# Kernel optimization log

Measured on AMD Instinct MI355X. Metric: run time of the kernel, lower is better.

Reference implementation:

```python
import jax, jax.numpy as jnp
import numpy as np

D_MODEL = 1024
NUM_HEADS = 16
HEAD_DIM = D_MODEL // NUM_HEADS


def setup_inputs() -> dict:
    key = jax.random.key(0)
    ks = jax.random.split(key, 5)
    scale = 0.02
    return {
        "x": jax.random.normal(ks[0], (1, 4096, D_MODEL), dtype=jnp.float32),
        "w_qkv": jax.random.normal(ks[1], (D_MODEL, 3 * D_MODEL), dtype=jnp.float32) * scale,
        "b_qkv": jax.random.normal(ks[2], (3 * D_MODEL,), dtype=jnp.float32) * scale,
        "w_out": jax.random.normal(ks[3], (D_MODEL, D_MODEL), dtype=jnp.float32) * scale,
        "b_out": jax.random.normal(ks[4], (D_MODEL,), dtype=jnp.float32) * scale,
    }


def reference(x, w_qkv, b_qkv, w_out, b_out):
    B, S, D = x.shape
    H, Hd = NUM_HEADS, HEAD_DIM
    qkv = x @ w_qkv + b_qkv  # [B,S,3D]
    q, k, v = jnp.split(qkv, 3, axis=-1)
    # [B,H,S,Hd]
    q = q.reshape(B, S, H, Hd).transpose(0, 2, 1, 3)
    k = k.reshape(B, S, H, Hd).transpose(0, 2, 1, 3)
    v = v.reshape(B, S, H, Hd).transpose(0, 2, 1, 3)
    scores = jnp.einsum("bhqd,bhkd->bhqk", q, k) / jnp.sqrt(jnp.float32(Hd))
    causal = jnp.tril(jnp.ones((S, S), dtype=bool))
    scores = jnp.where(causal[None, None, :, :], scores, -jnp.inf)
    attn = jax.nn.softmax(scores, axis=-1)  # dropout_p = 0.0 -> identity
    ctx = jnp.einsum("bhqk,bhkd->bhqd", attn, v)
    ctx = ctx.transpose(0, 2, 1, 3).reshape(B, S, D)
    return ctx @ w_out + b_out
```

## Files before the change

kernel.cpp:

```cpp
#include <hip/hip_runtime.h>

#define S 4096
#define DM 1024
#define NH 16
#define HD 64

typedef __attribute__((ext_vector_type(8))) short bf8;
typedef __attribute__((ext_vector_type(4))) float f4;
typedef __attribute__((ext_vector_type(4))) short s4;

#define MFMA __builtin_amdgcn_mfma_f32_16x16x32_bf16

#define QSCALE 0.18033688011112042f

static __device__ __forceinline__ unsigned short f2b(float f) {
  unsigned int u = __builtin_bit_cast(unsigned int, f);
  u += 0x7fffu + ((u >> 16) & 1u);
  return (unsigned short)(u >> 16);
}
static __device__ __forceinline__ float b2f(unsigned short u) {
  return __builtin_bit_cast(float, (unsigned int)u << 16);
}

static __device__ __forceinline__ void gld_lds(const unsigned short* g, unsigned short* l) {
  __builtin_amdgcn_global_load_lds(
      (const __attribute__((address_space(1))) unsigned int*)g,
      (__attribute__((address_space(3))) unsigned int*)l, 16, 0, 0);
}

__global__ void prep(const float* __restrict__ x, const float* __restrict__ w_qkv,
                     const float* __restrict__ w_out,
                     unsigned short* __restrict__ xb, unsigned short* __restrict__ wqkvT,
                     unsigned short* __restrict__ woutT) {
  __shared__ float tile[64][65];
  int b = blockIdx.x, t = threadIdx.x;
  if (b < 4096) {
    int i = (b * 256 + t) * 4;
    float4 v = *(const float4*)(x + i);
    s4 o;
    o.x = (short)f2b(v.x); o.y = (short)f2b(v.y);
    o.z = (short)f2b(v.z); o.w = (short)f2b(v.w);
    *(s4*)(xb + i) = o;
    return;
  }
  const float* in; unsigned short* out; int R, C, tc, tr;
  if (b < 4096 + 768) { int bb = b - 4096; in = w_qkv; out = wqkvT; R = DM; C = 3 * DM; tc = bb % 48; tr = bb / 48; }
  else                { int bb = b - 4864; in = w_out; out = woutT; R = DM; C = DM;     tc = bb % 16; tr = bb / 16; }
  int c = t & 63, rbase = (t >> 6) * 16;
#pragma unroll
  for (int i = 0; i < 16; i++) {
    int r = rbase + i;
    tile[r][c] = in[(tr * 64 + r) * C + tc * 64 + c];
  }
  __syncthreads();
#pragma unroll
  for (int i = 0; i < 16; i++) {
    int cc = rbase + i;
    out[(tc * 64 + cc) * R + tr * 64 + c] = f2b(tile[c][cc]);
  }
}


__global__ void __launch_bounds__(256, 2) gemm_qkv(const unsigned short* __restrict__ A,
                                                   const unsigned short* __restrict__ Bt,
                                                   const float* __restrict__ bias,
                                                   unsigned short* __restrict__ Qo,
                                                   unsigned short* __restrict__ Ko,
                                                   unsigned short* __restrict__ Vt) {
  __shared__ unsigned short lA[128 * 32];
  __shared__ unsigned short lB[128 * 32];
  int bid = blockIdx.x;
  int nb = bid % 24, mb = bid / 24;
  int m0 = mb * 128, n0 = nb * 128;
  int t = threadIdx.x, w = t >> 6, lane = t & 63;
  int col = lane & 15, quad = lane >> 4;
  int wm = (w >> 1) * 64, wn = (w & 1) * 64;

  int srow = lane >> 2;
  int sphys = lane & 3;

  f4 acc[4][4];
#pragma unroll
  for (int x = 0; x < 4; x++)
#pragma unroll
    for (int y = 0; y < 4; y++) acc[x][y] = (f4){0.f, 0.f, 0.f, 0.f};

  for (int k0 = 0; k0 < DM; k0 += 32) {
    __syncthreads();
#pragma unroll
    for (int p = 0; p < 2; p++) {
      int j = 2 * w + p;
      int row = j * 16 + srow;
      int lch = sphys ^ ((srow >> 1) & 3);
      gld_lds(A + (size_t)(m0 + row) * DM + k0 + lch * 8, lA + j * 512);
      gld_lds(Bt + (size_t)(n0 + row) * DM + k0 + lch * 8, lB + j * 512);
    }
    __syncthreads();

    bf8 af[4], bfr[4];
#pragma unroll
    for (int x = 0; x < 4; x++) {
      int rA = wm + x * 16 + col;
      af[x] = *(const bf8*)(lA + rA * 32 + (quad ^ ((col >> 1) & 3)) * 8);
      int rB = wn + x * 16 + col;
      bfr[x] = *(const bf8*)(lB + rB * 32 + (quad ^ ((col >> 1) & 3)) * 8);
    }
#pragma unroll
    for (int x = 0; x < 4; x++)
#pragma unroll
      for (int y = 0; y < 4; y++)
        acc[x][y] = MFMA(af[x], bfr[y], acc[x][y], 0, 0, 0);
  }

#pragma unroll
  for (int x = 0; x < 4; x++) {
    int s0r = m0 + wm + x * 16 + quad * 4;
#pragma unroll
    for (int y = 0; y < 4; y++) {
      f4 a = acc[x][y];
      int n = n0 + wn + y * 16 + col;
      float bv = bias[n];
      if (n < 2048) {
        unsigned short* dst = (n < 1024) ? Qo : Ko;
        float sc = (n < 1024) ? QSCALE : 1.0f;
        int nn = n & 1023;
        int hh = nn >> 6, d = nn & 63;
        unsigned short* pp = dst + ((size_t)hh * S + s0r) * HD + d;
#pragma unroll
        for (int r = 0; r < 4; r++) pp[r * HD] = f2b((a[r] + bv) * sc);
      } else {
        int nn = n - 2048;
        int hh = nn >> 6, d = nn & 63;
        s4 pk;
        pk.x = (short)f2b(a[0] + bv);
        pk.y = (short)f2b(a[1] + bv);
        pk.z = (short)f2b(a[2] + bv);
        pk.w = (short)f2b(a[3] + bv);
        *(s4*)(Vt + ((size_t)hh * HD + d) * S + s0r) = pk;
      }
    }
  }
}

__global__ void __launch_bounds__(256, 2) gemm_out(const unsigned short* __restrict__ A,
                                                   const unsigned short* __restrict__ Bt,
                                                   const float* __restrict__ bias,
                                                   float* __restrict__ out) {
  __shared__ unsigned short lA[128 * 32];
  __shared__ unsigned short lB[128 * 32];
  int bid = blockIdx.x;
  int nb = bid % 8, mb = bid / 8;
  int m0 = mb * 128, n0 = nb * 128;
  int t = threadIdx.x, w = t >> 6, lane = t & 63;
  int col = lane & 15, quad = lane >> 4;
  int wm = (w >> 1) * 64, wn = (w & 1) * 64;

  int srow = lane >> 2;
  int sphys = lane & 3;

  f4 acc[4][4];
#pragma unroll
  for (int x = 0; x < 4; x++)
#pragma unroll
    for (int y = 0; y < 4; y++) acc[x][y] = (f4){0.f, 0.f, 0.f, 0.f};

  for (int k0 = 0; k0 < DM; k0 += 32) {
    __syncthreads();
#pragma unroll
    for (int p = 0; p < 2; p++) {
      int j = 2 * w + p;
      int row = j * 16 + srow;
      int lch = sphys ^ ((srow >> 1) & 3);
      gld_lds(A + (size_t)(m0 + row) * DM + k0 + lch * 8, lA + j * 512);
      gld_lds(Bt + (size_t)(n0 + row) * DM + k0 + lch * 8, lB + j * 512);
    }
    __syncthreads();

    bf8 af[4], bfr[4];
#pragma unroll
    for (int x = 0; x < 4; x++) {
      int rA = wm + x * 16 + col;
      af[x] = *(const bf8*)(lA + rA * 32 + (quad ^ ((col >> 1) & 3)) * 8);
      int rB = wn + x * 16 + col;
      bfr[x] = *(const bf8*)(lB + rB * 32 + (quad ^ ((col >> 1) & 3)) * 8);
    }
#pragma unroll
    for (int x = 0; x < 4; x++)
#pragma unroll
      for (int y = 0; y < 4; y++)
        acc[x][y] = MFMA(af[x], bfr[y], acc[x][y], 0, 0, 0);
  }

#pragma unroll
  for (int x = 0; x < 4; x++) {
    int s0r = m0 + wm + x * 16 + quad * 4;
#pragma unroll
    for (int y = 0; y < 4; y++) {
      f4 a = acc[x][y];
      int n = n0 + wn + y * 16 + col;
      float bv = bias[n];
#pragma unroll
      for (int r = 0; r < 4; r++) out[(size_t)(s0r + r) * DM + n] = a[r] + bv;
    }
  }
}

__global__ void __launch_bounds__(256, 6) attn(const unsigned short* __restrict__ Q,
                                               const unsigned short* __restrict__ K,
                                               const unsigned short* __restrict__ Vt,
                                               unsigned short* __restrict__ slabA,
                                               unsigned short* __restrict__ slabB,
                                               float* __restrict__ lA_g,
                                               float* __restrict__ lB_g) {
  __shared__ unsigned short kbuf[64 * 64];
  __shared__ unsigned short vbuf[64 * 64];
  __shared__ unsigned short pbuf[4 * 16 * 72];

  int bid = blockIdx.x;
  int h = bid / 96;
  int r = 95 - (bid % 96);
  int qb, c0, nst, isB;
  if (r < 32) { qb = r; c0 = 0; nst = r + 1; isB = 0; }
  else {
    int qq = (r - 32) >> 1;
    qb = 32 + qq;
    int half = (r - 32) & 1;
    int ntot = qb + 1, nh = (ntot + 1) >> 1;
    if (half) { c0 = nh; nst = ntot - nh; isB = 1; }
    else      { c0 = 0;  nst = nh;       isB = 0; }
  }
  bool single = (qb < 32);
  int q0blk = qb * 64;
  int t = threadIdx.x, w = t >> 6, lane = t & 63;
  int col = lane & 15, quad = lane >> 4;
  int q0 = q0blk + w * 16;

  const unsigned short* Qh = Q + (size_t)h * S * HD;
  const unsigned short* Kh = K + (size_t)h * S * HD;
  const unsigned short* Vh = Vt + (size_t)h * HD * S;
  unsigned short* pl = pbuf + w * (16 * 72);

  bf8 qf0 = *(const bf8*)(Qh + (q0 + col) * HD + quad * 8);
  bf8 qf1 = *(const bf8*)(Qh + (q0 + col) * HD + 32 + quad * 8);

  f4 o[4];
#pragma unroll
  for (int dt = 0; dt < 4; dt++) o[dt] = (f4){0.f, 0.f, 0.f, 0.f};
  float lsum = 0.f;

  int srow = lane >> 3;
  int sphys = lane & 7;

  for (int s_ = 0; s_ < nst; s_++) {
    int kv0 = (c0 + s_) * 64;
    __syncthreads();
#pragma unroll
    for (int p = 0; p < 2; p++) {
      int j = 2 * w + p;
      int row = j * 8 + srow;
      int lch = sphys ^ (row & 7);
      gld_lds(Kh + (size_t)(kv0 + row) * HD + lch * 8, kbuf + j * 512);
      gld_lds(Vh + (size_t)row * S + kv0 + lch * 8, vbuf + j * 512);
    }
    __syncthreads();

    f4 st[4];
#pragma unroll
    for (int tt = 0; tt < 4; tt++) {
      int kr = tt * 16 + col;
      int sw = col & 7;
      bf8 ka = *(const bf8*)(kbuf + kr * 64 + (quad ^ sw) * 8);
      bf8 kb = *(const bf8*)(kbuf + kr * 64 + ((quad + 4) ^ sw) * 8);
      f4 z = {0.f, 0.f, 0.f, 0.f};
      z = MFMA(ka, qf0, z, 0, 0, 0);
      z = MFMA(kb, qf1, z, 0, 0, 0);
      st[tt] = z;
    }

    if (kv0 + 63 > q0) {
      int q = q0 + col;
#pragma unroll
      for (int tt = 0; tt < 4; tt++)
#pragma unroll
        for (int rr = 0; rr < 4; rr++) {
          int kv = kv0 + tt * 16 + quad * 4 + rr;
          st[tt][rr] = (kv <= q) ? st[tt][rr] : -1e30f;
        }
    }

#pragma unroll
    for (int tt = 0; tt < 4; tt++) {
      float p0 = __builtin_amdgcn_exp2f(st[tt][0]);
      float p1 = __builtin_amdgcn_exp2f(st[tt][1]);
      float p2 = __builtin_amdgcn_exp2f(st[tt][2]);
      float p3 = __builtin_amdgcn_exp2f(st[tt][3]);
      lsum += (p0 + p1) + (p2 + p3);
      s4 pk;
      pk.x = (short)f2b(p0); pk.y = (short)f2b(p1);
      pk.z = (short)f2b(p2); pk.w = (short)f2b(p3);
      *(s4*)((char*)pl + col * 144 + tt * 32 + quad * 8) = pk;
    }

    bf8 pf0 = *(const bf8*)(pl + col * 72 + quad * 8);
    bf8 pf1 = *(const bf8*)(pl + col * 72 + 32 + quad * 8);

#pragma unroll
    for (int dt = 0; dt < 4; dt++) {
      int vr = dt * 16 + col;
      int sw = col & 7;
      bf8 v0 = *(const bf8*)(vbuf + vr * 64 + (quad ^ sw) * 8);
      bf8 v1 = *(const bf8*)(vbuf + vr * 64 + ((quad + 4) ^ sw) * 8);
      o[dt] = MFMA(pf0, v0, o[dt], 0, 0, 0);
      o[dt] = MFMA(pf1, v1, o[dt], 0, 0, 0);
    }
  }

  lsum += __shfl_xor(lsum, 16);
  lsum += __shfl_xor(lsum, 32);

  if (single) {
    float inv = 1.0f / lsum;
    float ir[4];
#pragma unroll
    for (int rr = 0; rr < 4; rr++) ir[rr] = __shfl(inv, quad * 4 + rr);
#pragma unroll
    for (int dt = 0; dt < 4; dt++)
#pragma unroll
      for (int rr = 0; rr < 4; rr++) {
        int row = q0 + quad * 4 + rr;
        slabA[(size_t)row * DM + h * HD + dt * 16 + col] = f2b(o[dt][rr] * ir[rr]);
      }
  } else {
    unsigned short* slab = isB ? slabB : slabA;
    int rowbase = isB ? (q0 - 2048) : q0;
    float* lg = isB ? lB_g : lA_g;
    if (quad == 0) lg[h * S + q0 + col] = lsum;
#pragma unroll
    for (int dt = 0; dt < 4; dt++)
#pragma unroll
      for (int rr = 0; rr < 4; rr++) {
        int row = rowbase + quad * 4 + rr;
        slab[(size_t)row * DM + h * HD + dt * 16 + col] = f2b(o[dt][rr]);
      }
  }
}

__global__ void combine(unsigned short* __restrict__ Ctx,
                        const unsigned short* __restrict__ slabB,
                        const float* __restrict__ lA_g,
                        const float* __restrict__ lB_g) {
  int row = 2048 + blockIdx.x;
  int cc = threadIdx.x * 4;
  int h = cc >> 6;
  s4 a = *(const s4*)(Ctx + (size_t)row * DM + cc);
  s4 b = *(const s4*)(slabB + (size_t)(row - 2048) * DM + cc);
  float l = lA_g[h * S + row] + lB_g[h * S + row];
  float inv = 1.0f / l;
  s4 o;
  o.x = (short)f2b((b2f((unsigned short)a.x) + b2f((unsigned short)b.x)) * inv);
  o.y = (short)f2b((b2f((unsigned short)a.y) + b2f((unsigned short)b.y)) * inv);
  o.z = (short)f2b((b2f((unsigned short)a.z) + b2f((unsigned short)b.z)) * inv);
  o.w = (short)f2b((b2f((unsigned short)a.w) + b2f((unsigned short)b.w)) * inv);
  *(s4*)(Ctx + (size_t)row * DM + cc) = o;
}

extern "C" void kernel_launch(void* const* d_in, const int* in_sizes, int n_in,
                              void* d_out, int out_size, void* d_ws, size_t ws_size,
                              hipStream_t stream) {
  const float* x     = (const float*)d_in[0];
  const float* w_qkv = (const float*)d_in[1];
  const float* b_qkv = (const float*)d_in[2];
  const float* w_out = (const float*)d_in[3];
  const float* b_out = (const float*)d_in[4];
  float* out = (float*)d_out;

  char* ws = (char*)d_ws;
  unsigned short* xb    = (unsigned short*)(ws);
  unsigned short* wqkvT = (unsigned short*)(ws + (size_t)8  * 1048576);
  unsigned short* woutT = (unsigned short*)(ws + (size_t)14 * 1048576);
  unsigned short* Qb    = (unsigned short*)(ws + (size_t)16 * 1048576);
  unsigned short* Kb    = (unsigned short*)(ws + (size_t)24 * 1048576);
  unsigned short* Vtb   = (unsigned short*)(ws + (size_t)32 * 1048576);
  unsigned short* ctx   = (unsigned short*)(ws + (size_t)40 * 1048576);

  unsigned short* slabB = xb;
  float* lA_g = (float*)wqkvT;
  float* lB_g = (float*)(ws + (size_t)8 * 1048576 + 512 * 1024);

  prep<<<5120, 256, 0, stream>>>(x, w_qkv, w_out, xb, wqkvT, woutT);
  gemm_qkv<<<32 * 24, 256, 0, stream>>>(xb, wqkvT, b_qkv, Qb, Kb, Vtb);
  attn<<<NH * 96, 256, 0, stream>>>(Qb, Kb, Vtb, ctx, slabB, lA_g, lB_g);
  combine<<<2048, 256, 0, stream>>>(ctx, slabB, lA_g, lB_g);
  gemm_out<<<32 * 8, 256, 0, stream>>>(ctx, woutT, b_out, out);
}
```

Baseline: 219.2 us.

## Process two query subtiles per wave and build P fragments in registers via permlane swaps

The attention kernel drops from 4 waves to 2 waves per block, with each wave handling 32 query rows (two 16-row groups). This lets each K/V fragment read from LDS feed twice as many MFMAs. The P matrix no longer round-trips through a shared-memory buffer; it is packed with v_cvt_pk_bf16_f32 and rearranged across lanes with v_permlane32/16_swap to form the MFMA A operands directly. The cost is higher register pressure and fewer waves per block for hiding latency, and each thread now issues twice as many K/V global-to-LDS loads.

```diff
diff --git a/kernel.cpp b/kernel.cpp
--- a/kernel.cpp
+++ b/kernel.cpp
@@ -8,6 +8,7 @@
 typedef __attribute__((ext_vector_type(8))) short bf8;
 typedef __attribute__((ext_vector_type(4))) float f4;
 typedef __attribute__((ext_vector_type(4))) short s4;
+typedef __attribute__((ext_vector_type(4))) unsigned int u4;
 
 #define MFMA __builtin_amdgcn_mfma_f32_16x16x32_bf16
 
@@ -205,7 +206,7 @@
   }
 }
 
-__global__ void __launch_bounds__(256, 6) attn(const unsigned short* __restrict__ Q,
+__global__ void __launch_bounds__(128, 4) attn(const unsigned short* __restrict__ Q,
                                                const unsigned short* __restrict__ K,
                                                const unsigned short* __restrict__ Vt,
                                                unsigned short* __restrict__ slabA,
@@ -214,7 +215,6 @@
                                                float* __restrict__ lB_g) {
   __shared__ unsigned short kbuf[64 * 64];
   __shared__ unsigned short vbuf[64 * 64];
-  __shared__ unsigned short pbuf[4 * 16 * 72];
 
   int bid = blockIdx.x;
   int h = bid / 96;
@@ -233,20 +233,25 @@
   int q0blk = qb * 64;
   int t = threadIdx.x, w = t >> 6, lane = t & 63;
   int col = lane & 15, quad = lane >> 4;
-  int q0 = q0blk + w * 16;
+  int q0 = q0blk + w * 32;
 
   const unsigned short* Qh = Q + (size_t)h * S * HD;
   const unsigned short* Kh = K + (size_t)h * S * HD;
   const unsigned short* Vh = Vt + (size_t)h * HD * S;
-  unsigned short* pl = pbuf + w * (16 * 72);
-
-  bf8 qf0 = *(const bf8*)(Qh + (q0 + col) * HD + quad * 8);
-  bf8 qf1 = *(const bf8*)(Qh + (q0 + col) * HD + 32 + quad * 8);
-
-  f4 o[4];
-#pragma unroll
-  for (int dt = 0; dt < 4; dt++) o[dt] = (f4){0.f, 0.f, 0.f, 0.f};
-  float lsum = 0.f;
+
+  bf8 qf[2][2];
+#pragma unroll
+  for (int g = 0; g < 2; g++) {
+    qf[g][0] = *(const bf8*)(Qh + (q0 + g * 16 + col) * HD + quad * 8);
+    qf[g][1] = *(const bf8*)(Qh + (q0 + g * 16 + col) * HD + 32 + quad * 8);
+  }
+
+  f4 o[2][4];
+#pragma unroll
+  for (int g = 0; g < 2; g++)
+#pragma unroll
+    for (int dt = 0; dt < 4; dt++) o[g][dt] = (f4){0.f, 0.f, 0.f, 0.f};
+  float lsum[2] = {0.f, 0.f};
 
   int srow = lane >> 3;
   int sphys = lane & 7;
@@ -255,8 +260,8 @@
     int kv0 = (c0 + s_) * 64;
     __syncthreads();
 #pragma unroll
-    for (int p = 0; p < 2; p++) {
-      int j = 2 * w + p;
+    for (int p = 0; p < 4; p++) {
+      int j = 4 * w + p;
       int row = j * 8 + srow;
       int lch = sphys ^ (row & 7);
       gld_lds(Kh + (size_t)(kv0 + row) * HD + lch * 8, kbuf + j * 512);
@@ -264,45 +269,63 @@
     }
     __syncthreads();
 
-    f4 st[4];
+    f4 st[2][4];
 #pragma unroll
     for (int tt = 0; tt < 4; tt++) {
       int kr = tt * 16 + col;
       int sw = col & 7;
       bf8 ka = *(const bf8*)(kbuf + kr * 64 + (quad ^ sw) * 8);
       bf8 kb = *(const bf8*)(kbuf + kr * 64 + ((quad + 4) ^ sw) * 8);
-      f4 z = {0.f, 0.f, 0.f, 0.f};
-      z = MFMA(ka, qf0, z, 0, 0, 0);
-      z = MFMA(kb, qf1, z, 0, 0, 0);
-      st[tt] = z;
-    }
-
-    if (kv0 + 63 > q0) {
-      int q = q0 + col;
-#pragma unroll
-      for (int tt = 0; tt < 4; tt++)
-#pragma unroll
-        for (int rr = 0; rr < 4; rr++) {
-          int kv = kv0 + tt * 16 + quad * 4 + rr;
-          st[tt][rr] = (kv <= q) ? st[tt][rr] : -1e30f;
-        }
-    }
-
-#pragma unroll
-    for (int tt = 0; tt < 4; tt++) {
-      float p0 = __builtin_amdgcn_exp2f(st[tt][0]);
-      float p1 = __builtin_amdgcn_exp2f(st[tt][1]);
-      float p2 = __builtin_amdgcn_exp2f(st[tt][2]);
-      float p3 = __builtin_amdgcn_exp2f(st[tt][3]);
-      lsum += (p0 + p1) + (p2 + p3);
-      s4 pk;
-      pk.x = (short)f2b(p0); pk.y = (short)f2b(p1);
-      pk.z = (short)f2b(p2); pk.w = (short)f2b(p3);
-      *(s4*)((char*)pl + col * 144 + tt * 32 + quad * 8) = pk;
-    }
-
-    bf8 pf0 = *(const bf8*)(pl + col * 72 + quad * 8);
-    bf8 pf1 = *(const bf8*)(pl + col * 72 + 32 + quad * 8);
+#pragma unroll
+      for (int g = 0; g < 2; g++) {
+        f4 z = {0.f, 0.f, 0.f, 0.f};
+        z = MFMA(ka, qf[g][0], z, 0, 0, 0);
+        z = MFMA(kb, qf[g][1], z, 0, 0, 0);
+        st[g][tt] = z;
+      }
+    }
+
+#pragma unroll
+    for (int g = 0; g < 2; g++) {
+      int q16 = q0 + g * 16;
+      if (kv0 + 63 > q16) {
+        int q = q16 + col;
+#pragma unroll
+        for (int tt = 0; tt < 4; tt++)
+#pragma unroll
+          for (int rr = 0; rr < 4; rr++) {
+            int kv = kv0 + tt * 16 + quad * 4 + rr;
+            st[g][tt][rr] = (kv <= q) ? st[g][tt][rr] : -1e30f;
+          }
+      }
+    }
+
+    bf8 pf[2][2];
+#pragma unroll
+    for (int g = 0; g < 2; g++) {
+      float pv[4][4];
+#pragma unroll
+      for (int tt = 0; tt < 4; tt++) {
+#pragma unroll
+        for (int rr = 0; rr < 4; rr++) pv[tt][rr] = __builtin_amdgcn_exp2f(st[g][tt][rr]);
+        lsum[g] += (pv[tt][0] + pv[tt][1]) + (pv[tt][2] + pv[tt][3]);
+      }
+#pragma unroll
+      for (int f = 0; f < 2; f++) {
+        unsigned int a0, a1, b0, b1;
+        asm("v_cvt_pk_bf16_f32 %0, %1, %2" : "=v"(a0) : "v"(pv[2 * f][0]),     "v"(pv[2 * f][1]));
+        asm("v_cvt_pk_bf16_f32 %0, %1, %2" : "=v"(a1) : "v"(pv[2 * f][2]),     "v"(pv[2 * f][3]));
+        asm("v_cvt_pk_bf16_f32 %0, %1, %2" : "=v"(b0) : "v"(pv[2 * f + 1][0]), "v"(pv[2 * f + 1][1]));
+        asm("v_cvt_pk_bf16_f32 %0, %1, %2" : "=v"(b1) : "v"(pv[2 * f + 1][2]), "v"(pv[2 * f + 1][3]));
+        asm("v_permlane32_swap_b32 %0, %1" : "+v"(a0), "+v"(b0));
+        asm("v_permlane32_swap_b32 %0, %1" : "+v"(a1), "+v"(b1));
+        asm("v_permlane16_swap_b32 %0, %1" : "+v"(a0), "+v"(b0));
+        asm("v_permlane16_swap_b32 %0, %1" : "+v"(a1), "+v"(b1));
+        u4 pk;
+        pk.x = a0; pk.y = a1; pk.z = b0; pk.w = b1;
+        pf[g][f] = __builtin_bit_cast(bf8, pk);
+      }
+    }
 
 #pragma unroll
     for (int dt = 0; dt < 4; dt++) {
@@ -310,38 +333,45 @@
       int sw = col & 7;
       bf8 v0 = *(const bf8*)(vbuf + vr * 64 + (quad ^ sw) * 8);
       bf8 v1 = *(const bf8*)(vbuf + vr * 64 + ((quad + 4) ^ sw) * 8);
-      o[dt] = MFMA(pf0, v0, o[dt], 0, 0, 0);
-      o[dt] = MFMA(pf1, v1, o[dt], 0, 0, 0);
-    }
-  }
-
-  lsum += __shfl_xor(lsum, 16);
-  lsum += __shfl_xor(lsum, 32);
-
-  if (single) {
-    float inv = 1.0f / lsum;
-    float ir[4];
-#pragma unroll
-    for (int rr = 0; rr < 4; rr++) ir[rr] = __shfl(inv, quad * 4 + rr);
-#pragma unroll
-    for (int dt = 0; dt < 4; dt++)
-#pragma unroll
-      for (int rr = 0; rr < 4; rr++) {
-        int row = q0 + quad * 4 + rr;
-        slabA[(size_t)row * DM + h * HD + dt * 16 + col] = f2b(o[dt][rr] * ir[rr]);
-      }
-  } else {
-    unsigned short* slab = isB ? slabB : slabA;
-    int rowbase = isB ? (q0 - 2048) : q0;
-    float* lg = isB ? lB_g : lA_g;
-    if (quad == 0) lg[h * S + q0 + col] = lsum;
-#pragma unroll
-    for (int dt = 0; dt < 4; dt++)
-#pragma unroll
-      for (int rr = 0; rr < 4; rr++) {
-        int row = rowbase + quad * 4 + rr;
-        slab[(size_t)row * DM + h * HD + dt * 16 + col] = f2b(o[dt][rr]);
-      }
+#pragma unroll
+      for (int g = 0; g < 2; g++) {
+        o[g][dt] = MFMA(pf[g][0], v0, o[g][dt], 0, 0, 0);
+        o[g][dt] = MFMA(pf[g][1], v1, o[g][dt], 0, 0, 0);
+      }
+    }
+  }
+
+#pragma unroll
+  for (int g = 0; g < 2; g++) {
+    float ls = lsum[g];
+    ls += __shfl_xor(ls, 16);
+    ls += __shfl_xor(ls, 32);
+    int q16 = q0 + g * 16;
+    if (single) {
+      float inv = 1.0f / ls;
+      float ir[4];
+#pragma unroll
+      for (int rr = 0; rr < 4; rr++) ir[rr] = __shfl(inv, quad * 4 + rr);
+#pragma unroll
+      for (int dt = 0; dt < 4; dt++)
+#pragma unroll
+        for (int rr = 0; rr < 4; rr++) {
+          int row = q16 + quad * 4 + rr;
+          slabA[(size_t)row * DM + h * HD + dt * 16 + col] = f2b(o[g][dt][rr] * ir[rr]);
+        }
+    } else {
+      unsigned short* slab = isB ? slabB : slabA;
+      int rowbase = isB ? (q16 - 2048) : q16;
+      float* lg = isB ? lB_g : lA_g;
+      if (quad == 0) lg[h * S + q16 + col] = ls;
+#pragma unroll
+      for (int dt = 0; dt < 4; dt++)
+#pragma unroll
+        for (int rr = 0; rr < 4; rr++) {
+          int row = rowbase + quad * 4 + rr;
+          slab[(size_t)row * DM + h * HD + dt * 16 + col] = f2b(o[g][dt][rr]);
+        }
+    }
   }
 }
 
@@ -389,7 +419,7 @@
 
   prep<<<5120, 256, 0, stream>>>(x, w_qkv, w_out, xb, wqkvT, woutT);
   gemm_qkv<<<32 * 24, 256, 0, stream>>>(xb, wqkvT, b_qkv, Qb, Kb, Vtb);
-  attn<<<NH * 96, 256, 0, stream>>>(Qb, Kb, Vtb, ctx, slabB, lA_g, lB_g);
+  attn<<<NH * 96, 128, 0, stream>>>(Qb, Kb, Vtb, ctx, slabB, lA_g, lB_g);
   combine<<<2048, 256, 0, stream>>>(ctx, slabB, lA_g, lB_g);
   gemm_out<<<32 * 8, 256, 0, stream>>>(ctx, woutT, b_out, out);
 }
```

New measurement: 215.8 us. About the same (-1.6%).
